# Optimization experiments

Measured on AMD Instinct MI355X. Metric: run time of the kernel, lower is better.

Reference implementation:

```python
import jax, jax.numpy as jnp
import numpy as np
from jax import lax

EPS = 1e-5
NF, NH, HD = 1024, 2, 2  # num_features, heads, head_size (hidden_size=4)


def _prelu(x, a):
    return jnp.where(x >= 0, x, a * x)


def _bn2d(x, g, b):  # training-mode BatchNorm2d over (N,H,W)
    m = x.mean(axis=(0, 2, 3), keepdims=True)
    v = ((x - m) ** 2).mean(axis=(0, 2, 3), keepdims=True)
    return (x - m) / jnp.sqrt(v + EPS) * g[None, :, None, None] + b[None, :, None, None]


def _bn1d(x, g, b):  # training-mode BatchNorm1d over batch
    m = x.mean(axis=0, keepdims=True)
    v = ((x - m) ** 2).mean(axis=0, keepdims=True)
    return (x - m) / jnp.sqrt(v + EPS) * g + b


def _ln(x, g, b):
    m = x.mean(axis=-1, keepdims=True)
    v = ((x - m) ** 2).mean(axis=-1, keepdims=True)
    return (x - m) / jnp.sqrt(v + EPS) * g + b


def _conv(x, w, b, stride):
    y = lax.conv_general_dilated(x, w, window_strides=stride, padding='VALID',
                                 dimension_numbers=('NCHW', 'OIHW', 'NCHW'))
    return y + b[None, :, None, None]


def setup_inputs() -> dict:
    key = jax.random.key(0)
    ks = jax.random.split(key, 24)
    r = lambda i, shape, s=0.05: jax.random.normal(ks[i], shape, jnp.float32) * s
    ones = lambda n: jnp.ones((n,), jnp.float32)
    zeros = lambda n: jnp.zeros((n,), jnp.float32)
    return {
        'vertex_pos': r(0, (32, 3), 1.0),
        'body_mesh': r(1, (32, 20813, 3), 1.0),
        'conv1_w': r(2, (3, 1, 409, 3)), 'conv1_b': r(3, (3,)),
        'bn1_g': ones(3), 'bn1_b': zeros(3),
        'conv2_w': r(4, (3, 1, 330, 3)), 'conv2_b': r(5, (3,)),
        'bn2_g': ones(3), 'bn2_b': zeros(3),
        'prelu_a': jnp.float32(0.25),
        'wq': r(6, (4, 9)), 'bq': r(7, (4,)),
        'wk': r(8, (4, 9)), 'bk': r(9, (4,)),
        'wv': r(10, (4, 9)), 'bv': r(11, (4,)),
        'fc_w': r(12, (1024, 4096)), 'fc_b': r(13, (1024,)),
        'ff1_w': r(14, (1024, 1024)), 'ff1_b': r(15, (1024,)),
        'ln_g': ones(1024), 'ln_b': zeros(1024),
        'ff2_w': r(16, (48, 1024)), 'ff2_b': r(17, (48,)),
        'fus_w0': r(18, (48, 32, 3)), 'fus_b0': r(19, (48, 32)),
        'fus_w1': r(20, (48, 128, 32)), 'fus_b1': r(21, (48, 128)),
        'bnf0_g': ones(32), 'bnf0_b': zeros(32),
        'bnf1_g': ones(128), 'bnf1_b': zeros(128),
        'prelu_f': jnp.float32(0.25),
        'out_w': r(22, (1, 128)), 'out_b': r(23, (1,)),
    }


def reference(vertex_pos, body_mesh, conv1_w, conv1_b, bn1_g, bn1_b, conv2_w, conv2_b,
              bn2_g, bn2_b, prelu_a, wq, bq, wk, bk, wv, bv, fc_w, fc_b,
              ff1_w, ff1_b, ln_g, ln_b, ff2_w, ff2_b,
              fus_w0, fus_b0, fus_w1, fus_b1, bnf0_g, bnf0_b, bnf1_g, bnf1_b,
              prelu_f, out_w, out_b):
    B = vertex_pos.shape[0]
    # --- mesh encoder (MultiHeadAttention_conv.mesh_encoder) ---
    mesh = body_mesh.reshape(B, 1, -1, 3)                             # [B,1,20813,3]
    x = _bn2d(_conv(mesh, conv1_w, conv1_b, (6, 1)), bn1_g, bn1_b)    # [B,3,3401,1]
    x = x.reshape(B, 1, -1, 3)                                        # [B,1,3401,3]
    x = _bn2d(_conv(x, conv2_w, conv2_b, (1, 1)), bn2_g, bn2_b)       # [B,3,3072,1]
    x = _prelu(x.reshape(B, NF, -1), prelu_a)                         # [B,1024,9]
    # --- multi-head attention ---
    def heads(t):  # [B,NF,NH*HD] -> [B,NH,NF,HD]
        return t.reshape(B, NF, NH, HD).transpose(0, 2, 1, 3)
    q = heads(x @ wq.T + bq)
    k = heads(x @ wk.T + bk)
    v = heads(x @ wv.T + bv)
    scores = jnp.einsum('bhqd,bhkd->bhqk', q, k) / (HD ** 0.5)        # [B,2,1024,1024]
    attn = jax.nn.softmax(scores, axis=-1)
    av = jnp.einsum('bhqk,bhkd->bhqd', attn, v)
    av = av.transpose(0, 2, 1, 3).reshape(B, NF * NH * HD)            # [B,4096]
    h = av @ fc_w.T + fc_b                                            # [B,1024]
    # --- GMW feed-forward (residual) + motion weights ---
    h = h + jax.nn.elu(_ln(h @ ff1_w.T + ff1_b, ln_g, ln_b))
    mw = h @ ff2_w.T + ff2_b                                          # [B,48]
    w = mw / jnp.sum(mw, axis=1, keepdims=True)                       # normalized gates
    # --- fused MoE stage: 48 experts per depth, batched as one grouped GEMM ---
    s = vertex_pos.reshape(B, 3)
    for We, be, g, bb in ((fus_w0, fus_b0, bnf0_g, bnf0_b),
                          (fus_w1, fus_b1, bnf1_g, bnf1_b)):
        y = jnp.einsum('eoi,bi->beo', We, s) + be[None]               # [B,48,out]
        s = jnp.einsum('beo,be->bo', y, w)                            # gated sum over experts
        s = _prelu(_bn1d(s, g, bb), prelu_f)
    return jax.nn.sigmoid(s @ out_w.T + out_b)                        # [B,1]
```

## Files before the change

### kernel.cpp

```cpp
#include <hip/hip_runtime.h>

#define EPSF 1e-5f

__device__ __forceinline__ float wred(float v) {
#pragma unroll
  for (int off = 32; off > 0; off >>= 1) v += __shfl_down(v, off, 64);
  return v;
}

__global__ __launch_bounds__(256) void k_conv1(
    const float* __restrict__ mesh, const float* __restrict__ cw,
    const float* __restrict__ cb, float* __restrict__ out,
    float* __restrict__ part) {
  __shared__ float wT[3888];
  __shared__ float P[3672];
  __shared__ float red[3072];
  __shared__ float pm2[384];
  __shared__ float redm[4][6];
  const int tid = threadIdx.x;
  const int tile = blockIdx.x % 27, b = blockIdx.x / 27;
  const int oh0 = tile << 7;
  const int nvalid = min(128, 3401 - oh0);
  for (int j = tid; j < 3888; j += 256) {
    int c = j / 1296, rem = j - c * 1296;
    int u = rem / 72, t = rem - u * 72;
    int i = 18 * t + u;
    wT[j] = (i < 1227) ? cw[c * 1227 + i] : 0.f;
  }
  {
    const int zoff = oh0 * 18;
    const float* src = mesh + b * 62439;
    for (int j = tid; j < 3672; j += 256) {
      int p = j / 18, u = j - p * 18;
      int z = zoff + j;
      P[u * 204 + p] = (z < 62439) ? src[z] : 0.f;
    }
  }
  __syncthreads();
  const int kc = tid >> 5, s = tid & 31;
  const int xb = s << 2;
  const int nu = (kc < 2) ? 3 : 2;
  float acc[3][4] = {};
  for (int ui = 0; ui < nu; ++ui) {
    const int u = (ui == 0) ? kc : ((ui == 1) ? kc + 8 : kc + 16);
    const float* Pu = P + u * 204 + xb;
    const float* w0p = wT + u * 72;
    const float* w1p = wT + 1296 + u * 72;
    const float* w2p = wT + 2592 + u * 72;
    float4 cur = *(const float4*)(Pu);
    float4 nxt = *(const float4*)(Pu + 4);
#pragma unroll 6
    for (int tg = 0; tg < 72; tg += 4) {
      float4 wv0 = *(const float4*)(w0p + tg);
      float4 wv1 = *(const float4*)(w1p + tg);
      float4 wv2 = *(const float4*)(w2p + tg);
      float x0 = cur.x, x1 = cur.y, x2 = cur.z, x3 = cur.w;
      float x4 = nxt.x, x5 = nxt.y, x6 = nxt.z;
      acc[0][0] = fmaf(wv0.x, x0, fmaf(wv0.y, x1, fmaf(wv0.z, x2, fmaf(wv0.w, x3, acc[0][0]))));
      acc[0][1] = fmaf(wv0.x, x1, fmaf(wv0.y, x2, fmaf(wv0.z, x3, fmaf(wv0.w, x4, acc[0][1]))));
      acc[0][2] = fmaf(wv0.x, x2, fmaf(wv0.y, x3, fmaf(wv0.z, x4, fmaf(wv0.w, x5, acc[0][2]))));
      acc[0][3] = fmaf(wv0.x, x3, fmaf(wv0.y, x4, fmaf(wv0.z, x5, fmaf(wv0.w, x6, acc[0][3]))));
      acc[1][0] = fmaf(wv1.x, x0, fmaf(wv1.y, x1, fmaf(wv1.z, x2, fmaf(wv1.w, x3, acc[1][0]))));
      acc[1][1] = fmaf(wv1.x, x1, fmaf(wv1.y, x2, fmaf(wv1.z, x3, fmaf(wv1.w, x4, acc[1][1]))));
      acc[1][2] = fmaf(wv1.x, x2, fmaf(wv1.y, x3, fmaf(wv1.z, x4, fmaf(wv1.w, x5, acc[1][2]))));
      acc[1][3] = fmaf(wv1.x, x3, fmaf(wv1.y, x4, fmaf(wv1.z, x5, fmaf(wv1.w, x6, acc[1][3]))));
      acc[2][0] = fmaf(wv2.x, x0, fmaf(wv2.y, x1, fmaf(wv2.z, x2, fmaf(wv2.w, x3, acc[2][0]))));
      acc[2][1] = fmaf(wv2.x, x1, fmaf(wv2.y, x2, fmaf(wv2.z, x3, fmaf(wv2.w, x4, acc[2][1]))));
      acc[2][2] = fmaf(wv2.x, x2, fmaf(wv2.y, x3, fmaf(wv2.z, x4, fmaf(wv2.w, x5, acc[2][2]))));
      acc[2][3] = fmaf(wv2.x, x3, fmaf(wv2.y, x4, fmaf(wv2.z, x5, fmaf(wv2.w, x6, acc[2][3]))));
      cur = nxt;
      nxt = *(const float4*)(Pu + tg + 8);
    }
  }
#pragma unroll
  for (int r = 0; r < 4; ++r)
#pragma unroll
    for (int ch = 0; ch < 3; ++ch)
      red[kc * 384 + s * 12 + r * 3 + ch] = acc[ch][r];
  __syncthreads();
  float v0 = cb[tid % 3];
#pragma unroll
  for (int c2 = 0; c2 < 8; ++c2) v0 += red[c2 * 384 + tid];
  pm2[tid] = v0;
  if (tid < 128) {
    float v1 = cb[(tid + 256) % 3];
#pragma unroll
    for (int c2 = 0; c2 < 8; ++c2) v1 += red[c2 * 384 + tid + 256];
    pm2[tid + 256] = v1;
  }
  __syncthreads();
  float st[6] = {0.f, 0.f, 0.f, 0.f, 0.f, 0.f};
  if (tid < nvalid) {
    const int s2 = tid >> 2, r2 = tid & 3;
    float y0 = pm2[s2 * 12 + r2 * 3 + 0];
    float y1 = pm2[s2 * 12 + r2 * 3 + 1];
    float y2 = pm2[s2 * 12 + r2 * 3 + 2];
    float* op = out + b * 10203 + oh0 + tid;
    op[0] = y0; op[3401] = y1; op[6802] = y2;
    st[0] = y0; st[1] = y0 * y0; st[2] = y1; st[3] = y1 * y1; st[4] = y2; st[5] = y2 * y2;
  }
  const int lane = tid & 63, wid = tid >> 6;
#pragma unroll
  for (int c = 0; c < 6; ++c) {
    float rv = wred(st[c]);
    if (lane == 0) redm[wid][c] = rv;
  }
  __syncthreads();
  if (tid < 6)
    part[tid * 864 + blockIdx.x] = redm[0][tid] + redm[1][tid] + redm[2][tid] + redm[3][tid];
}

__global__ __launch_bounds__(256) void k_conv2(
    const float* __restrict__ x1, const float* __restrict__ part1,
    const float* __restrict__ g1, const float* __restrict__ be1,
    const float* __restrict__ cw, const float* __restrict__ cb,
    float* __restrict__ out, float* __restrict__ part) {
  __shared__ float wT[3024];
  __shared__ float P[3][852];
  __shared__ float red[1536];
  __shared__ float redm[4][6];
  __shared__ float coef[6];
  const int tid = threadIdx.x;
  const int lane = tid & 63, wid = tid >> 6;
  {
    float r6[6] = {0.f, 0.f, 0.f, 0.f, 0.f, 0.f};
    for (int j = tid; j < 864; j += 256) {
#pragma unroll
      for (int c = 0; c < 6; ++c) r6[c] += part1[c * 864 + j];
    }
#pragma unroll
    for (int c = 0; c < 6; ++c) {
      float rv = wred(r6[c]);
      if (lane == 0) redm[wid][c] = rv;
    }
    __syncthreads();
    if (tid == 0) {
      const float inv_n = 1.f / (32.f * 3401.f);
#pragma unroll
      for (int c = 0; c < 3; ++c) {
        float s = redm[0][2 * c] + redm[1][2 * c] + redm[2][2 * c] + redm[3][2 * c];
        float ss = redm[0][2 * c + 1] + redm[1][2 * c + 1] + redm[2][2 * c + 1] + redm[3][2 * c + 1];
        float m = s * inv_n;
        float var = ss * inv_n - m * m;
        float a = g1[c] * rsqrtf(var + EPSF);
        coef[c] = a; coef[3 + c] = be1[c] - m * a;
      }
    }
  }
  for (int j = tid; j < 3024; j += 256) {
    int u = j / 1008, rem = j - u * 1008;
    int c = rem / 336, t = rem - c * 336;
    wT[j] = (t < 330) ? cw[c * 990 + 3 * t + u] : 0.f;
  }
  __syncthreads();
  const int tile = blockIdx.x % 6, b = blockIdx.x / 6;
  const int oh0 = tile << 9;
  const int zbase = oh0 * 3;
  const float* src = x1 + b * 10203 + zbase;
  for (int j = tid; j < 2556; j += 256) {
    int rel = j / 3, u = j - rel * 3;
    float val = 0.f;
    int z = zbase + j;
    if (z <= 10202) {
      int c = (z >= 6802) ? 2 : ((z >= 3401) ? 1 : 0);
      val = fmaf(coef[c], src[j], coef[3 + c]);
    }
    P[u][rel] = val;
  }
  __syncthreads();
  const int kc = tid >> 7, s = tid & 127;
  const int t0 = kc * 168;
  const int xb = s << 2;
  float acc0[4] = {}, acc1[4] = {}, acc2[4] = {};
  float4 cur0 = *(const float4*)&P[0][xb + t0];
  float4 cur1 = *(const float4*)&P[1][xb + t0];
  float4 cur2 = *(const float4*)&P[2][xb + t0];
  float4 nxt0 = *(const float4*)&P[0][xb + t0 + 4];
  float4 nxt1 = *(const float4*)&P[1][xb + t0 + 4];
  float4 nxt2 = *(const float4*)&P[2][xb + t0 + 4];
  const int tend = t0 + 168;
  for (int tg = t0; tg < tend; tg += 4) {
#define CONV2_U(ACC0, ACC1, ACC2, UOFF, CUR, NXT)                                                  \
    {                                                                                              \
      const float* wu = wT + UOFF + tg;                                                            \
      float2 wa0 = *(const float2*)(wu);                                                           \
      float2 wb0 = *(const float2*)(wu + 2);                                                       \
      float2 wa1 = *(const float2*)(wu + 336);                                                     \
      float2 wb1 = *(const float2*)(wu + 338);                                                     \
      float2 wa2 = *(const float2*)(wu + 672);                                                     \
      float2 wb2 = *(const float2*)(wu + 674);                                                     \
      float x0 = CUR.x, x1v = CUR.y, x2v = CUR.z, x3v = CUR.w;                                     \
      float x4 = NXT.x, x5 = NXT.y, x6 = NXT.z;                                                    \
      ACC0[0] = fmaf(wa0.x, x0,  fmaf(wa0.y, x1v, fmaf(wb0.x, x2v, fmaf(wb0.y, x3v, ACC0[0]))));  \
      ACC0[1] = fmaf(wa0.x, x1v, fmaf(wa0.y, x2v, fmaf(wb0.x, x3v, fmaf(wb0.y, x4,  ACC0[1]))));  \
      ACC0[2] = fmaf(wa0.x, x2v, fmaf(wa0.y, x3v, fmaf(wb0.x, x4,  fmaf(wb0.y, x5,  ACC0[2]))));  \
      ACC0[3] = fmaf(wa0.x, x3v, fmaf(wa0.y, x4,  fmaf(wb0.x, x5,  fmaf(wb0.y, x6,  ACC0[3]))));  \
      ACC1[0] = fmaf(wa1.x, x0,  fmaf(wa1.y, x1v, fmaf(wb1.x, x2v, fmaf(wb1.y, x3v, ACC1[0]))));  \
      ACC1[1] = fmaf(wa1.x, x1v, fmaf(wa1.y, x2v, fmaf(wb1.x, x3v, fmaf(wb1.y, x4,  ACC1[1]))));  \
      ACC1[2] = fmaf(wa1.x, x2v, fmaf(wa1.y, x3v, fmaf(wb1.x, x4,  fmaf(wb1.y, x5,  ACC1[2]))));  \
      ACC1[3] = fmaf(wa1.x, x3v, fmaf(wa1.y, x4,  fmaf(wb1.x, x5,  fmaf(wb1.y, x6,  ACC1[3]))));  \
      ACC2[0] = fmaf(wa2.x, x0,  fmaf(wa2.y, x1v, fmaf(wb2.x, x2v, fmaf(wb2.y, x3v, ACC2[0]))));  \
      ACC2[1] = fmaf(wa2.x, x1v, fmaf(wa2.y, x2v, fmaf(wb2.x, x3v, fmaf(wb2.y, x4,  ACC2[1]))));  \
      ACC2[2] = fmaf(wa2.x, x2v, fmaf(wa2.y, x3v, fmaf(wb2.x, x4,  fmaf(wb2.y, x5,  ACC2[2]))));  \
      ACC2[3] = fmaf(wa2.x, x3v, fmaf(wa2.y, x4,  fmaf(wb2.x, x5,  fmaf(wb2.y, x6,  ACC2[3]))));  \
    }
    CONV2_U(acc0, acc1, acc2, 0,    cur0, nxt0)
    CONV2_U(acc0, acc1, acc2, 1008, cur1, nxt1)
    CONV2_U(acc0, acc1, acc2, 2016, cur2, nxt2)
#undef CONV2_U
    cur0 = nxt0; cur1 = nxt1; cur2 = nxt2;
    nxt0 = *(const float4*)&P[0][xb + tg + 8];
    nxt1 = *(const float4*)&P[1][xb + tg + 8];
    nxt2 = *(const float4*)&P[2][xb + tg + 8];
  }
  if (kc == 1) {
#pragma unroll
    for (int r = 0; r < 4; ++r) {
      red[s * 12 + r] = acc0[r];
      red[s * 12 + 4 + r] = acc1[r];
      red[s * 12 + 8 + r] = acc2[r];
    }
  }
  __syncthreads();
  float st[6] = {0.f, 0.f, 0.f, 0.f, 0.f, 0.f};
  if (kc == 0) {
    float y0[4], y1[4], y2[4];
#pragma unroll
    for (int r = 0; r < 4; ++r) {
      y0[r] = acc0[r] + red[s * 12 + r] + cb[0];
      y1[r] = acc1[r] + red[s * 12 + 4 + r] + cb[1];
      y2[r] = acc2[r] + red[s * 12 + 8 + r] + cb[2];
      st[0] += y0[r]; st[1] += y0[r] * y0[r];
      st[2] += y1[r]; st[3] += y1[r] * y1[r];
      st[4] += y2[r]; st[5] += y2[r] * y2[r];
    }
    float* op = out + b * 9216 + oh0 + xb;
    *(float4*)(op)        = make_float4(y0[0], y0[1], y0[2], y0[3]);
    *(float4*)(op + 3072) = make_float4(y1[0], y1[1], y1[2], y1[3]);
    *(float4*)(op + 6144) = make_float4(y2[0], y2[1], y2[2], y2[3]);
  }
#pragma unroll
  for (int c = 0; c < 6; ++c) {
    float rv = wred(st[c]);
    if (lane == 0) redm[wid][c] = rv;
  }
  __syncthreads();
  if (tid < 6)
    part[tid * 192 + blockIdx.x] = redm[0][tid] + redm[1][tid] + redm[2][tid] + redm[3][tid];
}

__global__ __launch_bounds__(256) void k_qkv(
    const float* __restrict__ x2, const float* __restrict__ part2,
    const float* __restrict__ g2, const float* __restrict__ be2,
    const float* __restrict__ pa_p,
    const float* __restrict__ wq, const float* __restrict__ bq,
    const float* __restrict__ wk, const float* __restrict__ bk,
    const float* __restrict__ wv, const float* __restrict__ bv,
    float* __restrict__ qo, float* __restrict__ ko, float* __restrict__ vo) {
  __shared__ float redm[4][6];
  __shared__ float coef[6];
  const int tid = threadIdx.x;
  const int lane = tid & 63, wid = tid >> 6;
  {
    float r[6] = {0.f, 0.f, 0.f, 0.f, 0.f, 0.f};
    for (int j = tid; j < 192; j += 256) {
#pragma unroll
      for (int c = 0; c < 6; ++c) r[c] += part2[c * 192 + j];
    }
#pragma unroll
    for (int c = 0; c < 6; ++c) {
      float rv = wred(r[c]);
      if (lane == 0) redm[wid][c] = rv;
    }
    __syncthreads();
    if (tid == 0) {
      const float inv_n = 1.f / (32.f * 3072.f);
#pragma unroll
      for (int c = 0; c < 3; ++c) {
        float s = redm[0][2 * c] + redm[1][2 * c] + redm[2][2 * c] + redm[3][2 * c];
        float ss = redm[0][2 * c + 1] + redm[1][2 * c + 1] + redm[2][2 * c + 1] + redm[3][2 * c + 1];
        float m = s * inv_n;
        float var = ss * inv_n - m * m;
        float a = g2[c] * rsqrtf(var + EPSF);
        coef[c] = a; coef[3 + c] = be2[c] - m * a;
      }
    }
    __syncthreads();
  }
  const float pa = pa_p[0];
  const int id = blockIdx.x * 256 + tid;
  const int b = id >> 10, f = id & 1023;
  const float* src = x2 + b * 9216 + f * 9;
  float x[9];
  const int z0 = f * 9;
#pragma unroll
  for (int j = 0; j < 9; ++j) {
    int z = z0 + j;
    int c = (z >= 6144) ? 2 : ((z >= 3072) ? 1 : 0);
    float v = fmaf(coef[c], src[j], coef[3 + c]);
    x[j] = (v >= 0.f) ? v : pa * v;
  }
  const float QSCALE = 0.70710678118654752f * 1.44269504088896341f;
#pragma unroll
  for (int dd = 0; dd < 4; ++dd) {
    float q = bq[dd], k = bk[dd], v = bv[dd];
#pragma unroll
    for (int j = 0; j < 9; ++j) {
      q = fmaf(wq[dd * 9 + j], x[j], q);
      k = fmaf(wk[dd * 9 + j], x[j], k);
      v = fmaf(wv[dd * 9 + j], x[j], v);
    }
    int hh = dd >> 1, d = dd & 1;
    int idx = ((b * 2 + hh) * 1024 + f) * 2 + d;
    qo[idx] = q * QSCALE;
    ko[idx] = k;
    vo[idx] = v;
  }
}

__device__ __forceinline__ int kvIdx(int j) { return j + (j >> 7); }

__global__ __launch_bounds__(256) void k_attn(
    const float* __restrict__ q, const float* __restrict__ k,
    const float* __restrict__ v, float* __restrict__ av) {
  __shared__ float4 kv[1032];
  __shared__ float smax[4];
  const int tid = threadIdx.x;
  const int bh = blockIdx.x >> 3, rblk = blockIdx.x & 7;
  const float2* kp = (const float2*)(k + bh * 2048);
  const float2* vp = (const float2*)(v + bh * 2048);
  float nkm = 0.f;
  for (int j = tid; j < 1024; j += 256) {
    float2 kk = kp[j], vv = vp[j];
    kv[kvIdx(j)] = make_float4(kk.x, kk.y, vv.x, vv.y);
    nkm = fmaxf(nkm, fmaf(kk.x, kk.x, kk.y * kk.y));
  }
#pragma unroll
  for (int off = 32; off > 0; off >>= 1) nkm = fmaxf(nkm, __shfl_xor(nkm, off, 64));
  if ((tid & 63) == 0) smax[tid >> 6] = nkm;
  __syncthreads();
  const float knorm = sqrtf(fmaxf(fmaxf(smax[0], smax[1]), fmaxf(smax[2], smax[3])));
  const int lane = tid & 63, w = tid >> 6;
  const int rg = (w << 3) | (lane >> 3);
  const int ks = lane & 7;
  const int r0 = rblk * 128 + rg * 4;
  const float4 q01 = *(const float4*)(q + (bh * 1024 + r0) * 2);
  const float4 q23 = *(const float4*)(q + (bh * 1024 + r0) * 2 + 4);
  float qx[4] = {q01.x, q01.z, q23.x, q23.z};
  float qy[4] = {q01.y, q01.w, q23.y, q23.w};
  float m[4], l[4] = {0.f, 0.f, 0.f, 0.f};
  float o0[4] = {0.f, 0.f, 0.f, 0.f}, o1[4] = {0.f, 0.f, 0.f, 0.f};
#pragma unroll
  for (int r = 0; r < 4; ++r) m[r] = sqrtf(fmaf(qx[r], qx[r], qy[r] * qy[r])) * knorm;
  const int j0 = ks * 128;
#pragma unroll 4
  for (int jj = 0; jj < 128; ++jj) {
    float4 kk = kv[kvIdx(j0 + jj)];
#pragma unroll
    for (int r = 0; r < 4; ++r) {
      float s = fmaf(qx[r], kk.x, qy[r] * kk.y);
      float p = exp2f(s - m[r]);
      l[r] += p;
      o0[r] = fmaf(p, kk.z, o0[r]);
      o1[r] = fmaf(p, kk.w, o1[r]);
    }
  }
#pragma unroll
  for (int off = 1; off <= 4; off <<= 1) {
#pragma unroll
    for (int r = 0; r < 4; ++r) {
      l[r] += __shfl_xor(l[r], off, 64);
      o0[r] += __shfl_xor(o0[r], off, 64);
      o1[r] += __shfl_xor(o1[r], off, 64);
    }
  }
  if (ks == 0) {
    const int b = bh >> 1, hh = bh & 1;
#pragma unroll
    for (int r = 0; r < 4; ++r) {
      float rl = 1.f / l[r];
      *(float2*)(av + b * 4096 + (r0 + r) * 4 + hh * 2) = make_float2(o0[r] * rl, o1[r] * rl);
    }
  }
}

__global__ __launch_bounds__(256) void k_fc(
    const float* __restrict__ x, const float* __restrict__ w,
    float* __restrict__ pout) {
  __shared__ float xs[128 * 36];
  const int tid = threadIdx.x;
  const int ob = blockIdx.x & 15, ksp = blockIdx.x >> 4;
  const int k0 = ksp * 128, obase = ob * 64;
  for (int r = tid; r < 4096; r += 256) {
    int b = r >> 7, kk = r & 127;
    xs[kk * 36 + b] = x[b * 4096 + k0 + kk];
  }
  __syncthreads();
  const int og = tid & 15, bg = tid >> 4;
  const int o = obase + og * 4, bb0 = bg * 2;
  float acc[4][2] = {};
  const float* wp = w + o * 4096 + k0;
  for (int kk = 0; kk < 128; kk += 4) {
    float2 x0 = *(const float2*)&xs[(kk + 0) * 36 + bb0];
    float2 x1 = *(const float2*)&xs[(kk + 1) * 36 + bb0];
    float2 x2 = *(const float2*)&xs[(kk + 2) * 36 + bb0];
    float2 x3 = *(const float2*)&xs[(kk + 3) * 36 + bb0];
#pragma unroll
    for (int oo = 0; oo < 4; ++oo) {
      float4 wv = *(const float4*)(wp + oo * 4096 + kk);
      acc[oo][0] = fmaf(wv.x, x0.x, fmaf(wv.y, x1.x, fmaf(wv.z, x2.x, fmaf(wv.w, x3.x, acc[oo][0]))));
      acc[oo][1] = fmaf(wv.x, x0.y, fmaf(wv.y, x1.y, fmaf(wv.z, x2.y, fmaf(wv.w, x3.y, acc[oo][1]))));
    }
  }
#pragma unroll
  for (int bi = 0; bi < 2; ++bi) {
    float4 rv = make_float4(acc[0][bi], acc[1][bi], acc[2][bi], acc[3][bi]);
    *(float4*)&pout[(ksp * 32 + bb0 + bi) * 1024 + o] = rv;
  }
}

__global__ __launch_bounds__(256) void k_hred(
    const float* __restrict__ pfc, const float* __restrict__ fcb,
    float* __restrict__ h) {
  const int idx = blockIdx.x * 256 + threadIdx.x;
  const int b = idx >> 10, o = idx & 1023;
  float hv = fcb[o];
#pragma unroll 4
  for (int j = 0; j < 32; ++j) hv += pfc[(j * 32 + b) * 1024 + o];
  h[idx] = hv;
}

__global__ __launch_bounds__(256) void k_ff1(
    const float* __restrict__ h, const float* __restrict__ w,
    float* __restrict__ pout) {
  __shared__ float xs[64 * 36];
  const int tid = threadIdx.x;
  const int ob = blockIdx.x & 15, ksp = blockIdx.x >> 4;
  const int k0 = ksp * 64, obase = ob * 64;
  for (int r = tid; r < 2048; r += 256) {
    int b = r >> 6, kk = r & 63;
    xs[kk * 36 + b] = h[b * 1024 + k0 + kk];
  }
  __syncthreads();
  const int og = tid & 15, bg = tid >> 4;
  const int o = obase + og * 4, bb0 = bg * 2;
  float acc[4][2] = {};
  const float* wp = w + o * 1024 + k0;
  for (int kk = 0; kk < 64; kk += 4) {
    float2 x0 = *(const float2*)&xs[(kk + 0) * 36 + bb0];
    float2 x1 = *(const float2*)&xs[(kk + 1) * 36 + bb0];
    float2 x2 = *(const float2*)&xs[(kk + 2) * 36 + bb0];
    float2 x3 = *(const float2*)&xs[(kk + 3) * 36 + bb0];
#pragma unroll
    for (int oo = 0; oo < 4; ++oo) {
      float4 wv = *(const float4*)(wp + oo * 1024 + kk);
      acc[oo][0] = fmaf(wv.x, x0.x, fmaf(wv.y, x1.x, fmaf(wv.z, x2.x, fmaf(wv.w, x3.x, acc[oo][0]))));
      acc[oo][1] = fmaf(wv.x, x0.y, fmaf(wv.y, x1.y, fmaf(wv.z, x2.y, fmaf(wv.w, x3.y, acc[oo][1]))));
    }
  }
#pragma unroll
  for (int bi = 0; bi < 2; ++bi) {
    float4 rv = make_float4(acc[0][bi], acc[1][bi], acc[2][bi], acc[3][bi]);
    *(float4*)&pout[(ksp * 32 + bb0 + bi) * 1024 + o] = rv;
  }
}

__global__ __launch_bounds__(256) void k_tail1(
    const float* __restrict__ h, const float* __restrict__ pff1,
    const float* __restrict__ ff1b,
    const float* __restrict__ lng, const float* __restrict__ lnb,
    const float* __restrict__ f2w, const float* __restrict__ f2b,
    const float* __restrict__ vp, const float* __restrict__ w0,
    const float* __restrict__ b0, float* __restrict__ wgate,
    float* __restrict__ s1pre) {
  __shared__ float hs[1024], ts[1024];
  __shared__ float mw_s[48];
  __shared__ float red2[4][2];
  __shared__ float bc[2];
  __shared__ float tot_s;
  const int b = blockIdx.x, tid = threadIdx.x;
  const int lane = tid & 63, wid = tid >> 6;
  for (int o = tid; o < 1024; o += 256) {
    hs[o] = h[b * 1024 + o];
    float tv = ff1b[o];
#pragma unroll 4
    for (int j = 0; j < 16; ++j) tv += pff1[(j * 32 + b) * 1024 + o];
    ts[o] = tv;
  }
  __syncthreads();
  float ls = 0.f, lss = 0.f;
  for (int o = tid; o < 1024; o += 256) {
    float t = ts[o];
    ls += t; lss += t * t;
  }
  ls = wred(ls); lss = wred(lss);
  if (lane == 0) { red2[wid][0] = ls; red2[wid][1] = lss; }
  __syncthreads();
  if (tid == 0) {
    float S = red2[0][0] + red2[1][0] + red2[2][0] + red2[3][0];
    float SS = red2[0][1] + red2[1][1] + red2[2][1] + red2[3][1];
    float m = S * (1.f / 1024.f);
    float var = SS * (1.f / 1024.f) - m * m;
    bc[0] = m; bc[1] = rsqrtf(var + EPSF);
  }
  __syncthreads();
  const float m = bc[0], inv = bc[1];
  for (int o = tid; o < 1024; o += 256) {
    float y = fmaf((ts[o] - m) * inv, lng[o], lnb[o]);
    float e = (y > 0.f) ? y : expm1f(y);
    ts[o] = hs[o] + e;
  }
  __syncthreads();
  if (tid < 192) {
    int e = tid >> 2, part = tid & 3;
    float acc = 0.f;
    const float* wr = f2w + e * 1024 + part * 4;
    for (int i = 0; i < 64; ++i) {
      float4 wv = *(const float4*)(wr + i * 16);
      int ob = i * 16 + part * 4;
      acc = fmaf(wv.x, ts[ob], fmaf(wv.y, ts[ob + 1], fmaf(wv.z, ts[ob + 2], fmaf(wv.w, ts[ob + 3], acc))));
    }
    acc += __shfl_down(acc, 1, 64);
    acc += __shfl_down(acc, 2, 64);
    if (part == 0) mw_s[e] = acc + f2b[e];
  }
  __syncthreads();
  if (tid < 64) {
    float v = (tid < 48) ? mw_s[tid] : 0.f;
    float t = wred(v);
    if (tid == 0) tot_s = t;
  }
  __syncthreads();
  if (tid < 48) {
    float wg = mw_s[tid] / tot_s;
    mw_s[tid] = wg;
    wgate[b * 48 + tid] = wg;
  }
  __syncthreads();
  if (tid < 32) {
    const int o = tid;
    const float v0 = vp[b * 3], v1 = vp[b * 3 + 1], v2 = vp[b * 3 + 2];
    float acc = 0.f;
#pragma unroll 4
    for (int e = 0; e < 48; ++e) {
      const float* wr = w0 + (e * 32 + o) * 3;
      float y = b0[e * 32 + o] + wr[0] * v0 + wr[1] * v1 + wr[2] * v2;
      acc = fmaf(mw_s[e], y, acc);
    }
    s1pre[b * 32 + o] = acc;
  }
}

__global__ __launch_bounds__(128) void k_moe1(
    const float* __restrict__ s1pre, const float* __restrict__ g0,
    const float* __restrict__ be0, const float* __restrict__ pf_p,
    const float* __restrict__ wgate, const float* __restrict__ w1,
    const float* __restrict__ b1, float* __restrict__ pmoe) {
  __shared__ float s1n[32];
  __shared__ float wgs[6];
  const int tid = threadIdx.x;
  const int b = blockIdx.x >> 3, ech = blockIdx.x & 7;
  const int e0 = ech * 6;
  const float pf = pf_p[0];
  if (tid < 6) wgs[tid] = wgate[b * 48 + e0 + tid];
  if (tid < 32) {
    const int o = tid;
    float s = 0.f, ss = 0.f;
    for (int bb = 0; bb < 32; ++bb) {
      float v = s1pre[bb * 32 + o];
      s += v; ss += v * v;
    }
    float mm = s * (1.f / 32.f);
    float var = ss * (1.f / 32.f) - mm * mm;
    float a = g0[o] * rsqrtf(var + EPSF);
    float c = be0[o] - mm * a;
    float v = fmaf(s1pre[b * 32 + o], a, c);
    s1n[o] = (v >= 0.f) ? v : pf * v;
  }
  __syncthreads();
  const int op = tid;
  float acc = 0.f;
#pragma unroll
  for (int ee = 0; ee < 6; ++ee) {
    const int e = e0 + ee;
    const float* wr = w1 + (e * 128 + op) * 32;
    float y = b1[e * 128 + op];
#pragma unroll
    for (int i = 0; i < 32; i += 4) {
      float4 wv = *(const float4*)(wr + i);
      y = fmaf(wv.x, s1n[i], fmaf(wv.y, s1n[i + 1], fmaf(wv.z, s1n[i + 2], fmaf(wv.w, s1n[i + 3], y))));
    }
    acc = fmaf(wgs[ee], y, acc);
  }
  pmoe[ech * 4096 + b * 128 + op] = acc;
}

__global__ __launch_bounds__(256) void k_final(
    const float* __restrict__ pmoe, const float* __restrict__ g1,
    const float* __restrict__ be1, const float* __restrict__ pf_p,
    const float* __restrict__ ow, const float* __restrict__ obp,
    float* __restrict__ outp) {
  __shared__ float s2[32 * 132];
  __shared__ float ca[128], cb[128];
  const int tid = threadIdx.x;
  for (int r = tid; r < 4096; r += 256) {
    int b = r >> 7, o = r & 127;
    float v = 0.f;
#pragma unroll
    for (int j = 0; j < 8; ++j) v += pmoe[j * 4096 + r];
    s2[b * 132 + o] = v;
  }
  __syncthreads();
  if (tid < 128) {
    const int o = tid;
    float s = 0.f, ss = 0.f;
    for (int b = 0; b < 32; ++b) {
      float v = s2[b * 132 + o];
      s += v; ss += v * v;
    }
    float mm = s * (1.f / 32.f);
    float var = ss * (1.f / 32.f) - mm * mm;
    float a = g1[o] * rsqrtf(var + EPSF);
    ca[o] = a; cb[o] = be1[o] - mm * a;
  }
  __syncthreads();
  const float pf = pf_p[0];
  if (tid < 32) {
    const int b = tid;
    float acc = 0.f;
#pragma unroll 4
    for (int o = 0; o < 128; ++o) {
      float v = fmaf(s2[b * 132 + o], ca[o], cb[o]);
      v = (v >= 0.f) ? v : pf * v;
      acc = fmaf(v, ow[o], acc);
    }
    float z = acc + obp[0];
    outp[b] = 1.f / (1.f + __expf(-z));
  }
}

extern "C" void kernel_launch(void* const* d_in, const int* in_sizes, int n_in,
                              void* d_out, int out_size, void* d_ws, size_t ws_size,
                              hipStream_t stream) {
  (void)in_sizes; (void)n_in; (void)out_size; (void)ws_size;
  const float* vertex_pos = (const float*)d_in[0];
  const float* body_mesh  = (const float*)d_in[1];
  const float* conv1_w    = (const float*)d_in[2];
  const float* conv1_b    = (const float*)d_in[3];
  const float* bn1_g      = (const float*)d_in[4];
  const float* bn1_b      = (const float*)d_in[5];
  const float* conv2_w    = (const float*)d_in[6];
  const float* conv2_b    = (const float*)d_in[7];
  const float* bn2_g      = (const float*)d_in[8];
  const float* bn2_b      = (const float*)d_in[9];
  const float* prelu_a    = (const float*)d_in[10];
  const float* wq = (const float*)d_in[11]; const float* bq = (const float*)d_in[12];
  const float* wk = (const float*)d_in[13]; const float* bk = (const float*)d_in[14];
  const float* wv = (const float*)d_in[15]; const float* bv = (const float*)d_in[16];
  const float* fc_w  = (const float*)d_in[17]; const float* fc_b  = (const float*)d_in[18];
  const float* ff1_w = (const float*)d_in[19]; const float* ff1_b = (const float*)d_in[20];
  const float* ln_g  = (const float*)d_in[21]; const float* ln_b  = (const float*)d_in[22];
  const float* ff2_w = (const float*)d_in[23]; const float* ff2_b = (const float*)d_in[24];
  const float* fus_w0 = (const float*)d_in[25]; const float* fus_b0 = (const float*)d_in[26];
  const float* fus_w1 = (const float*)d_in[27]; const float* fus_b1 = (const float*)d_in[28];
  const float* bnf0_g = (const float*)d_in[29]; const float* bnf0_b = (const float*)d_in[30];
  const float* bnf1_g = (const float*)d_in[31]; const float* bnf1_b = (const float*)d_in[32];
  const float* prelu_f = (const float*)d_in[33];
  const float* out_w = (const float*)d_in[34]; const float* out_b = (const float*)d_in[35];

  float* ws = (float*)d_ws;
  float* conv1_out = ws + 0;
  float* conv2_out = ws + 326496;
  float* qws = ws + 621408;
  float* kws = ws + 752480;
  float* vws = ws + 883552;
  float* p_fc = ws + 0;
  float* av    = ws + 1048576;
  float* hbuf  = ws + 1179648;
  float* p_ff1 = ws + 1212416;
  float* part1 = ws + 1736704;
  float* part2 = ws + 1741888;
  float* wgate = ws + 1746496;
  float* s1pre = ws + 1748032;
  float* pmoe  = ws + 1749056;

  k_conv1<<<864, 256, 0, stream>>>(body_mesh, conv1_w, conv1_b, conv1_out, part1);
  k_conv2<<<192, 256, 0, stream>>>(conv1_out, part1, bn1_g, bn1_b, conv2_w, conv2_b, conv2_out, part2);
  k_qkv<<<128, 256, 0, stream>>>(conv2_out, part2, bn2_g, bn2_b, prelu_a,
                                 wq, bq, wk, bk, wv, bv, qws, kws, vws);
  k_attn<<<512, 256, 0, stream>>>(qws, kws, vws, av);
  k_fc<<<512, 256, 0, stream>>>(av, fc_w, p_fc);
  k_hred<<<128, 256, 0, stream>>>(p_fc, fc_b, hbuf);
  k_ff1<<<256, 256, 0, stream>>>(hbuf, ff1_w, p_ff1);
  k_tail1<<<32, 256, 0, stream>>>(hbuf, p_ff1, ff1_b, ln_g, ln_b, ff2_w, ff2_b,
                                  vertex_pos, fus_w0, fus_b0, wgate, s1pre);
  k_moe1<<<256, 128, 0, stream>>>(s1pre, bnf0_g, bnf0_b, prelu_f, wgate, fus_w1, fus_b1, pmoe);
  k_final<<<1, 256, 0, stream>>>(pmoe, bnf1_g, bnf1_b, prelu_f, out_w, out_b, (float*)d_out);
}
```

Baseline: 323.8 us.

## Precompute conv1 weight transpose globally and widen conv1 tiles to 256 outputs

Moves the conv1 weight reorder into a separate prep kernel writing a global buffer, so each conv1 block no longer rebuilds it in shared memory. The inner loop reads weights through a wave-uniform index from global/scalar memory. Output tiles grow from 128 to 256 positions with 64 lanes per kernel-row group, which halves the block count and the partial statistics conv2 has to reduce. This adds an extra launch and relies on the weight loads being served efficiently from cache or scalar loads.

Measured after the change: 315.6 us. -2.5%, faster.

```diff
diff --git a/kernel.cpp b/kernel.cpp
--- a/kernel.cpp
+++ b/kernel.cpp
@@ -8,66 +8,69 @@
   return v;
 }
 
-__global__ __launch_bounds__(256) void k_conv1(
-    const float* __restrict__ mesh, const float* __restrict__ cw,
-    const float* __restrict__ cb, float* __restrict__ out,
-    float* __restrict__ part) {
-  __shared__ float wT[3888];
-  __shared__ float P[3672];
-  __shared__ float red[3072];
-  __shared__ float pm2[384];
-  __shared__ float redm[4][6];
-  const int tid = threadIdx.x;
-  const int tile = blockIdx.x % 27, b = blockIdx.x / 27;
-  const int oh0 = tile << 7;
-  const int nvalid = min(128, 3401 - oh0);
-  for (int j = tid; j < 3888; j += 256) {
+__global__ __launch_bounds__(256) void k_wprep(
+    const float* __restrict__ cw, float* __restrict__ wTg) {
+  const int j = blockIdx.x * 256 + threadIdx.x;
+  if (j < 3888) {
     int c = j / 1296, rem = j - c * 1296;
     int u = rem / 72, t = rem - u * 72;
     int i = 18 * t + u;
-    wT[j] = (i < 1227) ? cw[c * 1227 + i] : 0.f;
-  }
+    wTg[j] = (i < 1227) ? cw[c * 1227 + i] : 0.f;
+  }
+}
+
+__global__ __launch_bounds__(256) void k_conv1(
+    const float* __restrict__ mesh, const float* __restrict__ wTg,
+    const float* __restrict__ cb, float* __restrict__ out,
+    float* __restrict__ part) {
+  __shared__ float P[5976];
+  __shared__ float red[3072];
+  __shared__ float pm2[768];
+  __shared__ float redm[4][6];
+  const int tid = threadIdx.x;
+  const int tile = blockIdx.x % 14, b = blockIdx.x / 14;
+  const int oh0 = tile << 8;
+  const int nvalid = min(256, 3401 - oh0);
   {
     const int zoff = oh0 * 18;
-    const float* src = mesh + b * 62439;
-    for (int j = tid; j < 3672; j += 256) {
+    const float* src = mesh + b * 62439 + zoff;
+    const int zmax = 62439 - zoff;
+    for (int j = tid; j < 5976; j += 256) {
       int p = j / 18, u = j - p * 18;
-      int z = zoff + j;
-      P[u * 204 + p] = (z < 62439) ? src[z] : 0.f;
-    }
-  }
-  __syncthreads();
-  const int kc = tid >> 5, s = tid & 31;
+      P[u * 332 + p] = (j < zmax) ? src[j] : 0.f;
+    }
+  }
+  __syncthreads();
+  const int kc = __builtin_amdgcn_readfirstlane(tid >> 6);
+  const int s = tid & 63;
   const int xb = s << 2;
-  const int nu = (kc < 2) ? 3 : 2;
+  const int nu = (kc < 2) ? 5 : 4;
   float acc[3][4] = {};
   for (int ui = 0; ui < nu; ++ui) {
-    const int u = (ui == 0) ? kc : ((ui == 1) ? kc + 8 : kc + 16);
-    const float* Pu = P + u * 204 + xb;
-    const float* w0p = wT + u * 72;
-    const float* w1p = wT + 1296 + u * 72;
-    const float* w2p = wT + 2592 + u * 72;
+    const int u = (ui < 4) ? (kc * 4 + ui) : (16 + kc);
+    const float* Pu = P + u * 332 + xb;
+    const float* wg = wTg + u * 72;
     float4 cur = *(const float4*)(Pu);
     float4 nxt = *(const float4*)(Pu + 4);
-#pragma unroll 6
+#pragma unroll
     for (int tg = 0; tg < 72; tg += 4) {
-      float4 wv0 = *(const float4*)(w0p + tg);
-      float4 wv1 = *(const float4*)(w1p + tg);
-      float4 wv2 = *(const float4*)(w2p + tg);
+      float4 w0 = *(const float4*)(wg + tg);
+      float4 w1 = *(const float4*)(wg + 1296 + tg);
+      float4 w2 = *(const float4*)(wg + 2592 + tg);
       float x0 = cur.x, x1 = cur.y, x2 = cur.z, x3 = cur.w;
       float x4 = nxt.x, x5 = nxt.y, x6 = nxt.z;
-      acc[0][0] = fmaf(wv0.x, x0, fmaf(wv0.y, x1, fmaf(wv0.z, x2, fmaf(wv0.w, x3, acc[0][0]))));
-      acc[0][1] = fmaf(wv0.x, x1, fmaf(wv0.y, x2, fmaf(wv0.z, x3, fmaf(wv0.w, x4, acc[0][1]))));
-      acc[0][2] = fmaf(wv0.x, x2, fmaf(wv0.y, x3, fmaf(wv0.z, x4, fmaf(wv0.w, x5, acc[0][2]))));
-      acc[0][3] = fmaf(wv0.x, x3, fmaf(wv0.y, x4, fmaf(wv0.z, x5, fmaf(wv0.w, x6, acc[0][3]))));
-      acc[1][0] = fmaf(wv1.x, x0, fmaf(wv1.y, x1, fmaf(wv1.z, x2, fmaf(wv1.w, x3, acc[1][0]))));
-      acc[1][1] = fmaf(wv1.x, x1, fmaf(wv1.y, x2, fmaf(wv1.z, x3, fmaf(wv1.w, x4, acc[1][1]))));
-      acc[1][2] = fmaf(wv1.x, x2, fmaf(wv1.y, x3, fmaf(wv1.z, x4, fmaf(wv1.w, x5, acc[1][2]))));
-      acc[1][3] = fmaf(wv1.x, x3, fmaf(wv1.y, x4, fmaf(wv1.z, x5, fmaf(wv1.w, x6, acc[1][3]))));
-      acc[2][0] = fmaf(wv2.x, x0, fmaf(wv2.y, x1, fmaf(wv2.z, x2, fmaf(wv2.w, x3, acc[2][0]))));
-      acc[2][1] = fmaf(wv2.x, x1, fmaf(wv2.y, x2, fmaf(wv2.z, x3, fmaf(wv2.w, x4, acc[2][1]))));
-      acc[2][2] = fmaf(wv2.x, x2, fmaf(wv2.y, x3, fmaf(wv2.z, x4, fmaf(wv2.w, x5, acc[2][2]))));
-      acc[2][3] = fmaf(wv2.x, x3, fmaf(wv2.y, x4, fmaf(wv2.z, x5, fmaf(wv2.w, x6, acc[2][3]))));
+      acc[0][0] = fmaf(w0.x, x0, fmaf(w0.y, x1, fmaf(w0.z, x2, fmaf(w0.w, x3, acc[0][0]))));
+      acc[0][1] = fmaf(w0.x, x1, fmaf(w0.y, x2, fmaf(w0.z, x3, fmaf(w0.w, x4, acc[0][1]))));
+      acc[0][2] = fmaf(w0.x, x2, fmaf(w0.y, x3, fmaf(w0.z, x4, fmaf(w0.w, x5, acc[0][2]))));
+      acc[0][3] = fmaf(w0.x, x3, fmaf(w0.y, x4, fmaf(w0.z, x5, fmaf(w0.w, x6, acc[0][3]))));
+      acc[1][0] = fmaf(w1.x, x0, fmaf(w1.y, x1, fmaf(w1.z, x2, fmaf(w1.w, x3, acc[1][0]))));
+      acc[1][1] = fmaf(w1.x, x1, fmaf(w1.y, x2, fmaf(w1.z, x3, fmaf(w1.w, x4, acc[1][1]))));
+      acc[1][2] = fmaf(w1.x, x2, fmaf(w1.y, x3, fmaf(w1.z, x4, fmaf(w1.w, x5, acc[1][2]))));
+      acc[1][3] = fmaf(w1.x, x3, fmaf(w1.y, x4, fmaf(w1.z, x5, fmaf(w1.w, x6, acc[1][3]))));
+      acc[2][0] = fmaf(w2.x, x0, fmaf(w2.y, x1, fmaf(w2.z, x2, fmaf(w2.w, x3, acc[2][0]))));
+      acc[2][1] = fmaf(w2.x, x1, fmaf(w2.y, x2, fmaf(w2.z, x3, fmaf(w2.w, x4, acc[2][1]))));
+      acc[2][2] = fmaf(w2.x, x2, fmaf(w2.y, x3, fmaf(w2.z, x4, fmaf(w2.w, x5, acc[2][2]))));
+      acc[2][3] = fmaf(w2.x, x3, fmaf(w2.y, x4, fmaf(w2.z, x5, fmaf(w2.w, x6, acc[2][3]))));
       cur = nxt;
       nxt = *(const float4*)(Pu + tg + 8);
     }
@@ -76,25 +79,22 @@
   for (int r = 0; r < 4; ++r)
 #pragma unroll
     for (int ch = 0; ch < 3; ++ch)
-      red[kc * 384 + s * 12 + r * 3 + ch] = acc[ch][r];
-  __syncthreads();
-  float v0 = cb[tid % 3];
-#pragma unroll
-  for (int c2 = 0; c2 < 8; ++c2) v0 += red[c2 * 384 + tid];
-  pm2[tid] = v0;
-  if (tid < 128) {
-    float v1 = cb[(tid + 256) % 3];
-#pragma unroll
-    for (int c2 = 0; c2 < 8; ++c2) v1 += red[c2 * 384 + tid + 256];
-    pm2[tid + 256] = v1;
+      red[kc * 768 + (xb + r) * 3 + ch] = acc[ch][r];
+  __syncthreads();
+#pragma unroll
+  for (int q = 0; q < 3; ++q) {
+    const int combo = q * 256 + tid;
+    float v = cb[combo % 3];
+#pragma unroll
+    for (int c2 = 0; c2 < 4; ++c2) v += red[c2 * 768 + combo];
+    pm2[combo] = v;
   }
   __syncthreads();
   float st[6] = {0.f, 0.f, 0.f, 0.f, 0.f, 0.f};
   if (tid < nvalid) {
-    const int s2 = tid >> 2, r2 = tid & 3;
-    float y0 = pm2[s2 * 12 + r2 * 3 + 0];
-    float y1 = pm2[s2 * 12 + r2 * 3 + 1];
-    float y2 = pm2[s2 * 12 + r2 * 3 + 2];
+    float y0 = pm2[tid * 3 + 0];
+    float y1 = pm2[tid * 3 + 1];
+    float y2 = pm2[tid * 3 + 2];
     float* op = out + b * 10203 + oh0 + tid;
     op[0] = y0; op[3401] = y1; op[6802] = y2;
     st[0] = y0; st[1] = y0 * y0; st[2] = y1; st[3] = y1 * y1; st[4] = y2; st[5] = y2 * y2;
@@ -107,7 +107,7 @@
   }
   __syncthreads();
   if (tid < 6)
-    part[tid * 864 + blockIdx.x] = redm[0][tid] + redm[1][tid] + redm[2][tid] + redm[3][tid];
+    part[tid * 448 + blockIdx.x] = redm[0][tid] + redm[1][tid] + redm[2][tid] + redm[3][tid];
 }
 
 __global__ __launch_bounds__(256) void k_conv2(
@@ -124,9 +124,9 @@
   const int lane = tid & 63, wid = tid >> 6;
   {
     float r6[6] = {0.f, 0.f, 0.f, 0.f, 0.f, 0.f};
-    for (int j = tid; j < 864; j += 256) {
-#pragma unroll
-      for (int c = 0; c < 6; ++c) r6[c] += part1[c * 864 + j];
+    for (int j = tid; j < 448; j += 256) {
+#pragma unroll
+      for (int c = 0; c < 6; ++c) r6[c] += part1[c * 448 + j];
     }
 #pragma unroll
     for (int c = 0; c < 6; ++c) {
@@ -683,8 +683,10 @@
   float* wgate = ws + 1746496;
   float* s1pre = ws + 1748032;
   float* pmoe  = ws + 1749056;
-
-  k_conv1<<<864, 256, 0, stream>>>(body_mesh, conv1_w, conv1_b, conv1_out, part1);
+  float* wTg   = ws + 1781824;
+
+  k_wprep<<<16, 256, 0, stream>>>(conv1_w, wTg);
+  k_conv1<<<448, 256, 0, stream>>>(body_mesh, wTg, conv1_b, conv1_out, part1);
   k_conv2<<<192, 256, 0, stream>>>(conv1_out, part1, bn1_g, bn1_b, conv2_w, conv2_b, conv2_out, part2);
   k_qkv<<<128, 256, 0, stream>>>(conv2_out, part2, bn2_g, bn2_b, prelu_a,
                                  wq, bq, wk, bk, wv, bv, qws, kws, vws);
```
